# Performance work log

Measured on AMD Instinct MI355X. Metric: run time of the kernel, lower is better.

## Reference

```python
import jax, jax.numpy as jnp
import numpy as np

N = 50000   # nodes
E = 800000  # edges
IND = 128   # in_dim
HID = 128   # num_hidden
NH = 4      # heads
HD = HID // NH
L = 2       # num_layers
SLOPE = 0.2


def setup_inputs() -> dict:
    key = jax.random.key(0)
    ks = jax.random.split(key, 32)
    rn = lambda k, shp, s=1.0: jax.random.normal(k, shp, jnp.float32) * s
    W = 0.08  # weight scale (xavier-ish)
    return {
        "x_t": rn(ks[0], (N, IND)),
        "time_embed": rn(ks[1], (N, HID)),
        "src": jax.random.randint(ks[2], (E,), 0, N),
        "dst": jax.random.randint(ks[3], (E,), 0, N),
        "W_init": rn(ks[4], (IND + HID, HID), W), "b_init": jnp.zeros((HID,), jnp.float32),
        "Wsrc_down": rn(ks[5], (L, HID, HID), W), "bsrc_down": jnp.zeros((L, HID), jnp.float32),
        "Wdst_down": rn(ks[6], (L, HID, HID), W), "bdst_down": jnp.zeros((L, HID), jnp.float32),
        "attn_down": rn(ks[7], (L, NH, HD), W), "bout_down": jnp.zeros((L, HID), jnp.float32),
        "Wsrc_mid": rn(ks[8], (HID, HID), W), "bsrc_mid": jnp.zeros((HID,), jnp.float32),
        "Wdst_mid": rn(ks[9], (HID, HID), W), "bdst_mid": jnp.zeros((HID,), jnp.float32),
        "attn_mid": rn(ks[10], (NH, HD), W), "bout_mid": jnp.zeros((HID,), jnp.float32),
        "Wsrc_up": rn(ks[11], (L, 2 * HID, HID), W), "bsrc_up": jnp.zeros((L, HID), jnp.float32),
        "Wdst_up": rn(ks[12], (L, 2 * HID, HID), W), "bdst_up": jnp.zeros((L, HID), jnp.float32),
        "attn_up": rn(ks[13], (L, NH, HD), W), "bout_up": jnp.zeros((L, HID), jnp.float32),
        "W_fin": rn(ks[14], (HID, HID), W), "b_fin": jnp.zeros((HID,), jnp.float32),
    }


def gatv2_layer(h, Wsrc, bsrc, Wdst, bdst, attn, bout, src, dst):
    # GATv2Conv (DGL semantics, eval mode / no dropout), flatten(1) included.
    fs = (h @ Wsrc + bsrc).reshape(-1, NH, HD)  # [N,H,D]
    fd = (h @ Wdst + bdst).reshape(-1, NH, HD)
    e = jax.nn.leaky_relu(fs[src] + fd[dst], SLOPE)           # [E,H,D]
    logits = jnp.einsum('ehd,hd->eh', e, attn)                # [E,H]
    m = jax.ops.segment_max(logits, dst, num_segments=N)      # [N,H]
    m = jnp.where(jnp.isfinite(m), m, 0.0)                    # zero-in-degree safety
    p = jnp.exp(logits - m[dst])                              # [E,H]
    s = jax.ops.segment_sum(p, dst, num_segments=N)           # [N,H]
    alpha = p / (s[dst] + 1e-9)                               # edge softmax per dst
    out = jax.ops.segment_sum(alpha[:, :, None] * fs[src], dst, num_segments=N)
    out = out.reshape(-1, HID) + bout
    return jax.nn.gelu(out)


def reference(x_t, time_embed, src, dst,
              W_init, b_init,
              Wsrc_down, bsrc_down, Wdst_down, bdst_down, attn_down, bout_down,
              Wsrc_mid, bsrc_mid, Wdst_mid, bdst_mid, attn_mid, bout_mid,
              Wsrc_up, bsrc_up, Wdst_up, bdst_up, attn_up, bout_up,
              W_fin, b_fin):
    h = jnp.concatenate([x_t, time_embed], axis=1)
    h = jax.nn.gelu(h @ W_init + b_init)
    skips = []
    for i in range(L):
        skips.append(h)
        h = gatv2_layer(h, Wsrc_down[i], bsrc_down[i], Wdst_down[i], bdst_down[i],
                        attn_down[i], bout_down[i], src, dst)
    h = gatv2_layer(h, Wsrc_mid, bsrc_mid, Wdst_mid, bdst_mid, attn_mid, bout_mid, src, dst)
    for i in range(L):
        h = jnp.concatenate([h, skips[L - 1 - i]], axis=1)
        h = gatv2_layer(h, Wsrc_up[i], bsrc_up[i], Wdst_up[i], bdst_up[i],
                        attn_up[i], bout_up[i], src, dst)
    out = h @ W_fin + b_fin
    return (out, h)
```

## Files before the change

kernel.cpp:

```cpp
#include <hip/hip_runtime.h>
#include <hip/hip_bf16.h>
#include <math.h>

#define HIDDIM 128

typedef float f32x4 __attribute__((ext_vector_type(4)));
typedef int i32x4 __attribute__((ext_vector_type(4)));
typedef short bf16x8 __attribute__((ext_vector_type(8)));

__device__ inline float gelu_f(float x) {
  float x3 = x * x * x;
  return 0.5f * x * (1.0f + tanhf(0.7978845608028654f * (x + 0.044715f * x3)));
}

__device__ inline void split_bf16(float a, unsigned short& hi, unsigned short& lo) {
  unsigned u = __float_as_uint(a);
  unsigned r = (u + 0x7FFFu + ((u >> 16) & 1u)) & 0xFFFF0000u;
  hi = (unsigned short)(r >> 16);
  float rem = a - __uint_as_float(r);
  unsigned u2 = __float_as_uint(rem);
  lo = (unsigned short)((u2 + 0x7FFFu + ((u2 >> 16) & 1u)) >> 16);
}

__device__ inline void split_pair(float a0, float a1, unsigned& hp, unsigned& lp) {
  unsigned u0 = __float_as_uint(a0), u1 = __float_as_uint(a1);
  unsigned r0 = (u0 + 0x7FFFu + ((u0 >> 16) & 1u)) & 0xFFFF0000u;
  unsigned r1 = (u1 + 0x7FFFu + ((u1 >> 16) & 1u)) & 0xFFFF0000u;
  hp = (r0 >> 16) | r1;
  float m0 = a0 - __uint_as_float(r0);
  float m1 = a1 - __uint_as_float(r1);
  unsigned v0 = __float_as_uint(m0), v1 = __float_as_uint(m1);
  unsigned s0 = v0 + 0x7FFFu + ((v0 >> 16) & 1u);
  unsigned s1 = (v1 + 0x7FFFu + ((v1 >> 16) & 1u)) & 0xFFFF0000u;
  lp = (s0 >> 16) | s1;
}

__global__ void detect_dtype(const unsigned short* __restrict__ raw, int* __restrict__ flag) {
  __shared__ int cnt;
  if (threadIdx.x == 0) cnt = 0;
  __syncthreads();
  int c = 0;
  for (int i = threadIdx.x; i < 8192; i += 256) {
    int ex = (raw[i] >> 7) & 0xFF;
    if (ex >= 0xC0) c++;
  }
  atomicAdd(&cnt, c);
  __syncthreads();
  if (threadIdx.x == 0) flag[0] = (cnt > 64) ? 1 : 0;
}

__global__ void cvt_to_f32_2(const void* __restrict__ in0, const void* __restrict__ in1,
                             float* __restrict__ out0, float* __restrict__ out1,
                             int n, const int* __restrict__ flag) {
  int i = blockIdx.x * 256 + threadIdx.x;
  if (i < n) {
    out0[i] = flag[0] ? ((const float*)in0)[i]
                      : __bfloat162float(((const __hip_bfloat16*)in0)[i]);
  } else if (i < 2 * n) {
    int j = i - n;
    out1[j] = flag[0] ? ((const float*)in1)[j]
                      : __bfloat162float(((const __hip_bfloat16*)in1)[j]);
  }
}

#define NITEMS 14
struct StageArgs {
  const void* src[NITEMS];
  int off[NITEMS];
  int n[NITEMS];
  int blk0[NITEMS];
};
__global__ void stage_params(StageArgs a, float* __restrict__ params,
                             const int* __restrict__ flag) {
  int b = blockIdx.x;
  int it = 0;
  while (it + 1 < NITEMS && a.blk0[it + 1] <= b) ++it;
  int i = (b - a.blk0[it]) * 256 + threadIdx.x;
  if (i < a.n[it]) {
    params[a.off[it] + i] = flag[0]
        ? ((const float*)a.src[it])[i]
        : __bfloat162float(((const __hip_bfloat16*)a.src[it])[i]);
  }
}

#define NSPLIT 12
struct SplitArgs {
  const void* src[NSPLIT];
  int eoff[NSPLIT];
  int soff[NSPLIT];
  int K[NSPLIT];
  int blk0[NSPLIT];
};
__global__ void split_weights(SplitArgs a,
                              unsigned short* __restrict__ whi,
                              unsigned short* __restrict__ wlo,
                              const int* __restrict__ flag) {
  int b = blockIdx.x, it = 0;
  while (it + 1 < NSPLIT && a.blk0[it + 1] <= b) ++it;
  int i = (b - a.blk0[it]) * 256 + threadIdx.x;
  int K = a.K[it];
  if (i < K * 128) {
    float v = flag[0]
        ? ((const float*)a.src[it])[a.eoff[it] + i]
        : __bfloat162float(((const __hip_bfloat16*)a.src[it])[a.eoff[it] + i]);
    int k = i >> 7, col = i & 127;
    unsigned short h, lo;
    split_bf16(v, h, lo);
    int o = a.soff[it] + col * K + k;
    whi[o] = h;
    wlo[o] = lo;
  }
}

template <int FUSED, int FINAL, int ACT, int ACCUM, int KS>
__global__ __launch_bounds__(256, 2) void gemm_ws(
    const float* __restrict__ A,
    const unsigned short* __restrict__ Whi0, const unsigned short* __restrict__ Wlo0,
    const unsigned short* __restrict__ Whi1, const unsigned short* __restrict__ Wlo1,
    const float* __restrict__ b0, const float* __restrict__ b1,
    float* __restrict__ C0, float* __restrict__ C1, int M) {
  constexpr int CT = FUSED ? 4 : 2;
  const int t = threadIdx.x;
  const int w = t >> 6, l = t & 63;
  const int lr = l & 15, lk = l >> 4;
  const unsigned short* whi = Whi0;
  const unsigned short* wlo = Wlo0;
  const float* bw = b0;
  float* Cw = C0;
  int cbase;
  if (FUSED) {
    if (w >> 1) { whi = Whi1; wlo = Wlo1; bw = b1; Cw = C1; }
    cbase = (w & 1) * 64;
  } else {
    cbase = w * 32;
  }

  bf16x8 wh[CT][4], wl[CT][4];
#pragma unroll
  for (int ct = 0; ct < CT; ++ct)
#pragma unroll
    for (int s = 0; s < 4; ++s) {
      size_t off = (size_t)(cbase + ct * 16 + lr) * KS + s * 32 + lk * 8;
      wh[ct][s] = *(const bf16x8*)&whi[off];
      wl[ct][s] = *(const bf16x8*)&wlo[off];
    }

  f32x4 bias[CT];
  if (FINAL) {
#pragma unroll
    for (int ct = 0; ct < CT; ++ct)
      bias[ct] = *(const f32x4*)&bw[cbase + ct * 16 + lk * 4];
  }

  const int ntiles = (M + 31) >> 5;
  for (int tb = blockIdx.x; tb < ntiles; tb += gridDim.x) {
    int row[2];
#pragma unroll
    for (int rt = 0; rt < 2; ++rt) row[rt] = min(tb * 32 + rt * 16 + lr, M - 1);

    float4 raw[2][4][2];
#pragma unroll
    for (int rt = 0; rt < 2; ++rt)
#pragma unroll
      for (int s = 0; s < 4; ++s) {
        const float* ap = &A[(size_t)row[rt] * 128 + s * 32 + lk * 8];
        raw[rt][s][0] = *(const float4*)ap;
        raw[rt][s][1] = *(const float4*)(ap + 4);
      }

    f32x4 acc[2][CT];
#pragma unroll
    for (int rt = 0; rt < 2; ++rt)
#pragma unroll
      for (int ct = 0; ct < CT; ++ct) acc[rt][ct] = (f32x4){0.f, 0.f, 0.f, 0.f};

#pragma unroll
    for (int s = 0; s < 4; ++s) {
      bf16x8 ah[2], al[2];
#pragma unroll
      for (int rt = 0; rt < 2; ++rt) {
        float4 v0 = raw[rt][s][0], v1 = raw[rt][s][1];
        i32x4 hv, lv;
        unsigned hp, lp;
        split_pair(v0.x, v0.y, hp, lp); hv[0] = (int)hp; lv[0] = (int)lp;
        split_pair(v0.z, v0.w, hp, lp); hv[1] = (int)hp; lv[1] = (int)lp;
        split_pair(v1.x, v1.y, hp, lp); hv[2] = (int)hp; lv[2] = (int)lp;
        split_pair(v1.z, v1.w, hp, lp); hv[3] = (int)hp; lv[3] = (int)lp;
        ah[rt] = __builtin_bit_cast(bf16x8, hv);
        al[rt] = __builtin_bit_cast(bf16x8, lv);
      }
#pragma unroll
      for (int rt = 0; rt < 2; ++rt)
#pragma unroll
        for (int ct = 0; ct < CT; ++ct) {
          acc[rt][ct] = __builtin_amdgcn_mfma_f32_16x16x32_bf16(wh[ct][s], ah[rt], acc[rt][ct], 0, 0, 0);
          acc[rt][ct] = __builtin_amdgcn_mfma_f32_16x16x32_bf16(wh[ct][s], al[rt], acc[rt][ct], 0, 0, 0);
          acc[rt][ct] = __builtin_amdgcn_mfma_f32_16x16x32_bf16(wl[ct][s], ah[rt], acc[rt][ct], 0, 0, 0);
        }
    }

#pragma unroll
    for (int rt = 0; rt < 2; ++rt) {
      int r = tb * 32 + rt * 16 + lr;
      if (r < M) {
        float* cp = &Cw[(size_t)r * 128 + cbase + lk * 4];
#pragma unroll
        for (int ct = 0; ct < CT; ++ct) {
          f32x4 v = acc[rt][ct];
          if (ACCUM) v += *(const f32x4*)(cp + ct * 16);
          if (FINAL) v += bias[ct];
          if (ACT) {
            v[0] = gelu_f(v[0]); v[1] = gelu_f(v[1]);
            v[2] = gelu_f(v[2]); v[3] = gelu_f(v[3]);
          }
          *(f32x4*)(cp + ct * 16) = v;
        }
      }
    }
  }
}

__global__ void count_deg(const int* __restrict__ dst, int* __restrict__ deg, int E) {
  int e = blockIdx.x * 256 + threadIdx.x;
  if (e < E) atomicAdd(&deg[dst[e]], 1);
}

__global__ __launch_bounds__(1024) void scan_blocks(
    const int* __restrict__ deg, int* __restrict__ rowptr,
    int* __restrict__ cursor, int* __restrict__ bsum, int N) {
  __shared__ int buf[1024];
  int i = blockIdx.x * 1024 + threadIdx.x;
  int v = (i < N) ? deg[i] : 0;
  buf[threadIdx.x] = v;
  __syncthreads();
  for (int off = 1; off < 1024; off <<= 1) {
    int add = (threadIdx.x >= (unsigned)off) ? buf[threadIdx.x - off] : 0;
    __syncthreads();
    buf[threadIdx.x] += add;
    __syncthreads();
  }
  int excl = buf[threadIdx.x] - v;
  if (i < N) { rowptr[i] = excl; cursor[i] = excl; }
  if (threadIdx.x == 1023) bsum[blockIdx.x] = buf[1023];
}

__global__ __launch_bounds__(1024) void scan_partials(int* __restrict__ bsum, int nb) {
  __shared__ int buf[1024];
  int v = (threadIdx.x < (unsigned)nb) ? bsum[threadIdx.x] : 0;
  buf[threadIdx.x] = v;
  __syncthreads();
  for (int off = 1; off < 1024; off <<= 1) {
    int add = (threadIdx.x >= (unsigned)off) ? buf[threadIdx.x - off] : 0;
    __syncthreads();
    buf[threadIdx.x] += add;
    __syncthreads();
  }
  int excl = buf[threadIdx.x] - v;
  if (threadIdx.x < (unsigned)nb) bsum[threadIdx.x] = excl;
  if (threadIdx.x == 1023) bsum[nb] = buf[1023];
}

__global__ void add_offsets(int* __restrict__ rowptr, int* __restrict__ cursor,
                            const int* __restrict__ bsum, int N, int nb) {
  int i = blockIdx.x * 256 + threadIdx.x;
  if (i < N) {
    int add = bsum[i >> 10];
    rowptr[i] += add;
    cursor[i] += add;
  }
  if (i == 0) rowptr[N] = bsum[nb];
}

__global__ void place_edges(const int* __restrict__ src, const int* __restrict__ dst,
                            int* __restrict__ cursor, int* __restrict__ colsrc, int E) {
  int e = blockIdx.x * 256 + threadIdx.x;
  if (e < E) {
    int pos = atomicAdd(&cursor[dst[e]], 1);
    colsrc[pos] = src[e];
  }
}

__global__ __launch_bounds__(256) void gat_agg(
    const float* __restrict__ fs, const float* __restrict__ fd,
    const int* __restrict__ rowptr, const int* __restrict__ colsrc,
    const float* __restrict__ attn, const float* __restrict__ bout,
    float* __restrict__ hout, int N, int E) {
  int wv = threadIdx.x >> 6, lane = threadIdx.x & 63;
  int n = blockIdx.x * 4 + wv;
  if (n >= N) return;
  int half = lane >> 5;
  int fb = (lane & 31) * 4;
  float4 fdv = *(const float4*)&fd[(size_t)n * HIDDIM + fb];
  float a0 = attn[fb], a1 = attn[fb + 1], a2 = attn[fb + 2], a3 = attn[fb + 3];
  int e0 = rowptr[n], e1 = rowptr[n + 1];
  e0 = max(0, min(e0, E));
  e1 = max(e0, min(e1, E));
  float s = 0.f, ax = 0.f, ay = 0.f, az = 0.f, aw = 0.f;
  for (int c0 = e0; c0 < e1; c0 += 64) {
    int cn = min(64, e1 - c0);
    int myidx = (lane < cn) ? colsrc[c0 + lane] : 0;
    myidx = ((unsigned)myidx < (unsigned)N) ? myidx : 0;
    int iters = (cn + 3) >> 2;
    for (int it = 0; it < iters; ++it) {
      int jA = 4 * it + half;
      int jB = jA + 2;
      int sA = __shfl(myidx, min(jA, cn - 1));
      int sB = __shfl(myidx, min(jB, cn - 1));
      float4 fA = *(const float4*)&fs[(size_t)sA * HIDDIM + fb];
      float4 fB = *(const float4*)&fs[(size_t)sB * HIDDIM + fb];
      float v0, v1, v2, v3, lA, lB;
      v0 = fA.x + fdv.x; v0 = v0 > 0.f ? v0 : 0.2f * v0;
      v1 = fA.y + fdv.y; v1 = v1 > 0.f ? v1 : 0.2f * v1;
      v2 = fA.z + fdv.z; v2 = v2 > 0.f ? v2 : 0.2f * v2;
      v3 = fA.w + fdv.w; v3 = v3 > 0.f ? v3 : 0.2f * v3;
      lA = fmaf(v0, a0, fmaf(v1, a1, fmaf(v2, a2, v3 * a3)));
      v0 = fB.x + fdv.x; v0 = v0 > 0.f ? v0 : 0.2f * v0;
      v1 = fB.y + fdv.y; v1 = v1 > 0.f ? v1 : 0.2f * v1;
      v2 = fB.z + fdv.z; v2 = v2 > 0.f ? v2 : 0.2f * v2;
      v3 = fB.w + fdv.w; v3 = v3 > 0.f ? v3 : 0.2f * v3;
      lB = fmaf(v0, a0, fmaf(v1, a1, fmaf(v2, a2, v3 * a3)));
      lA += __shfl_xor(lA, 1); lA += __shfl_xor(lA, 2); lA += __shfl_xor(lA, 4);
      lB += __shfl_xor(lB, 1); lB += __shfl_xor(lB, 2); lB += __shfl_xor(lB, 4);
      lA = fminf(lA, 60.f);
      lB = fminf(lB, 60.f);
      float pA = (jA < cn) ? __expf(lA) : 0.f;
      float pB = (jB < cn) ? __expf(lB) : 0.f;
      s += pA + pB;
      ax = fmaf(pA, fA.x, fmaf(pB, fB.x, ax));
      ay = fmaf(pA, fA.y, fmaf(pB, fB.y, ay));
      az = fmaf(pA, fA.z, fmaf(pB, fB.z, az));
      aw = fmaf(pA, fA.w, fmaf(pB, fB.w, aw));
    }
  }
  s += __shfl_xor(s, 32);
  ax += __shfl_xor(ax, 32); ay += __shfl_xor(ay, 32);
  az += __shfl_xor(az, 32); aw += __shfl_xor(aw, 32);
  if (half == 0) {
    float inv = 1.f / (s + 1e-9f);
    float o0 = gelu_f(fmaf(ax, inv, bout[fb]));
    float o1 = gelu_f(fmaf(ay, inv, bout[fb + 1]));
    float o2 = gelu_f(fmaf(az, inv, bout[fb + 2]));
    float o3 = gelu_f(fmaf(aw, inv, bout[fb + 3]));
    *(float4*)&hout[(size_t)n * HIDDIM + fb] = make_float4(o0, o1, o2, o3);
  }
}

__global__ void store_out(const float* __restrict__ og, const float* __restrict__ h,
                          void* __restrict__ dout, int n, const int* __restrict__ flag) {
  int i = blockIdx.x * 256 + threadIdx.x;
  if (i >= n) return;
  if (flag[0]) {
    ((float*)dout)[i] = og[i];
    ((float*)dout)[n + i] = h[i];
  } else {
    ((__hip_bfloat16*)dout)[i] = __float2bfloat16(og[i]);
    ((__hip_bfloat16*)dout)[n + i] = __float2bfloat16(h[i]);
  }
}

#define PB_INIT    0
#define PBSRC_DOWN 128
#define PBDST_DOWN 384
#define PATTN_DOWN 640
#define PBOUT_DOWN 896
#define PBSRC_MID  1152
#define PBDST_MID  1280
#define PATTN_MID  1408
#define PBOUT_MID  1536
#define PBSRC_UP   1664
#define PBDST_UP   1920
#define PATTN_UP   2176
#define PBOUT_UP   2432
#define PB_FIN     2688
#define PARAMS_TOTAL 2816

#define SP_W_INIT    0
#define SP_WSRC_D0   32768
#define SP_WSRC_D1   49152
#define SP_WDST_D0   65536
#define SP_WDST_D1   81920
#define SP_WSRC_MID  98304
#define SP_WDST_MID  114688
#define SP_WSRC_U0   131072
#define SP_WSRC_U1   163840
#define SP_WDST_U0   196608
#define SP_WDST_U1   229376
#define SP_W_FIN     262144
#define SPLIT_TOTAL  278528

extern "C" void kernel_launch(void* const* d_in, const int* in_sizes, int n_in,
                              void* d_out, int out_size, void* d_ws, size_t ws_size,
                              hipStream_t stream) {
  const int N = in_sizes[1] / HIDDIM;
  const int E = in_sizes[2];
  const int* src = (const int*)d_in[2];
  const int* dst = (const int*)d_in[3];

  char* p = (char*)d_ws;
  auto carve = [&](size_t bytes) {
    void* r = (void*)p;
    p += (bytes + 255) & ~(size_t)255;
    return r;
  };
  int* flag     = (int*)carve(256);
  float* params = (float*)carve((size_t)PARAMS_TOTAL * 4);
  unsigned short* whi = (unsigned short*)carve((size_t)SPLIT_TOTAL * 2);
  unsigned short* wlo = (unsigned short*)carve((size_t)SPLIT_TOTAL * 2);
  int* deg      = (int*)carve((size_t)N * 4);
  int* rowptr   = (int*)carve((size_t)(N + 1) * 4);
  int* cursor   = (int*)carve((size_t)N * 4);
  int* bsum     = (int*)carve(1032 * 4);
  int* colsrc   = (int*)carve((size_t)E * 4);
  float* hA     = (float*)carve((size_t)N * HIDDIM * 4);
  float* hB     = (float*)carve((size_t)N * HIDDIM * 4);
  float* hC     = (float*)carve((size_t)N * HIDDIM * 4);
  float* fs     = (float*)carve((size_t)N * HIDDIM * 4);
  float* fd     = (float*)carve((size_t)N * HIDDIM * 4);

  detect_dtype<<<1, 256, 0, stream>>>((const unsigned short*)d_in[0], flag);

  static const int idx[NITEMS] = {5, 7, 9, 10, 11, 13, 15, 16, 17, 19, 21, 22, 23, 25};
  static const int off[NITEMS] = {
    PB_INIT, PBSRC_DOWN, PBDST_DOWN, PATTN_DOWN, PBOUT_DOWN,
    PBSRC_MID, PBDST_MID, PATTN_MID, PBOUT_MID,
    PBSRC_UP, PBDST_UP, PATTN_UP, PBOUT_UP, PB_FIN};
  static const int cnt[NITEMS] = {
    128, 256, 256, 256, 256, 128, 128, 128, 128, 256, 256, 256, 256, 128};
  StageArgs sa;
  int nb = 0;
  for (int i = 0; i < NITEMS; ++i) {
    sa.src[i] = d_in[idx[i]];
    sa.off[i] = off[i];
    sa.n[i] = cnt[i];
    sa.blk0[i] = nb;
    nb += (cnt[i] + 255) / 256;
  }
  stage_params<<<nb, 256, 0, stream>>>(sa, params, flag);

  static const int widx[NSPLIT]  = {4, 6, 6, 8, 8, 12, 14, 18, 18, 20, 20, 24};
  static const int weoff[NSPLIT] = {0, 0, 16384, 0, 16384, 0, 0, 0, 32768, 0, 32768, 0};
  static const int wsoff[NSPLIT] = {
    SP_W_INIT, SP_WSRC_D0, SP_WSRC_D1, SP_WDST_D0, SP_WDST_D1,
    SP_WSRC_MID, SP_WDST_MID, SP_WSRC_U0, SP_WSRC_U1, SP_WDST_U0, SP_WDST_U1,
    SP_W_FIN};
  static const int wK[NSPLIT] = {256, 128, 128, 128, 128, 128, 128, 256, 256, 256, 256, 128};
  SplitArgs spa;
  int snb = 0;
  for (int i = 0; i < NSPLIT; ++i) {
    spa.src[i] = d_in[widx[i]];
    spa.eoff[i] = weoff[i];
    spa.soff[i] = wsoff[i];
    spa.K[i] = wK[i];
    spa.blk0[i] = snb;
    snb += (wK[i] * 128 + 255) / 256;
  }
  split_weights<<<snb, 256, 0, stream>>>(spa, whi, wlo, flag);

  float* xc = fs;
  float* tc = fd;
  cvt_to_f32_2<<<(2 * N * HIDDIM + 255) / 256, 256, 0, stream>>>(
      d_in[0], d_in[1], xc, tc, N * HIDDIM, flag);

  hipMemsetAsync(deg, 0, (size_t)N * 4, stream);
  count_deg<<<(E + 255) / 256, 256, 0, stream>>>(dst, deg, E);
  int nsb = (N + 1023) / 1024;
  scan_blocks<<<nsb, 1024, 0, stream>>>(deg, rowptr, cursor, bsum, N);
  scan_partials<<<1, 1024, 0, stream>>>(bsum, nsb);
  add_offsets<<<(N + 255) / 256, 256, 0, stream>>>(rowptr, cursor, bsum, N, nsb);
  place_edges<<<(E + 255) / 256, 256, 0, stream>>>(src, dst, cursor, colsrc, E);

  const int ntiles = (N + 31) >> 5;
  dim3 gw((unsigned)min(512, ntiles));
  dim3 ga((N + 3) / 4);
  const float* P = params;
  const unsigned short* nh = nullptr;

  gemm_ws<0, 0, 0, 0, 256><<<gw, 256, 0, stream>>>(
      xc, whi + SP_W_INIT, wlo + SP_W_INIT, nh, nh,
      nullptr, nullptr, hA, nullptr, N);
  gemm_ws<0, 1, 1, 1, 256><<<gw, 256, 0, stream>>>(
      tc, whi + SP_W_INIT + 128, wlo + SP_W_INIT + 128, nh, nh,
      P + PB_INIT, nullptr, hA, nullptr, N);

  gemm_ws<1, 1, 0, 0, 128><<<gw, 256, 0, stream>>>(
      hA, whi + SP_WSRC_D0, wlo + SP_WSRC_D0, whi + SP_WDST_D0, wlo + SP_WDST_D0,
      P + PBSRC_DOWN, P + PBDST_DOWN, fs, fd, N);
  gat_agg<<<ga, 256, 0, stream>>>(fs, fd, rowptr, colsrc,
                                  P + PATTN_DOWN, P + PBOUT_DOWN, hB, N, E);
  gemm_ws<1, 1, 0, 0, 128><<<gw, 256, 0, stream>>>(
      hB, whi + SP_WSRC_D1, wlo + SP_WSRC_D1, whi + SP_WDST_D1, wlo + SP_WDST_D1,
      P + PBSRC_DOWN + 128, P + PBDST_DOWN + 128, fs, fd, N);
  gat_agg<<<ga, 256, 0, stream>>>(fs, fd, rowptr, colsrc,
                                  P + PATTN_DOWN + 128, P + PBOUT_DOWN + 128, hC, N, E);
  gemm_ws<1, 1, 0, 0, 128><<<gw, 256, 0, stream>>>(
      hC, whi + SP_WSRC_MID, wlo + SP_WSRC_MID, whi + SP_WDST_MID, wlo + SP_WDST_MID,
      P + PBSRC_MID, P + PBDST_MID, fs, fd, N);
  gat_agg<<<ga, 256, 0, stream>>>(fs, fd, rowptr, colsrc,
                                  P + PATTN_MID, P + PBOUT_MID, hC, N, E);
  gemm_ws<1, 0, 0, 0, 256><<<gw, 256, 0, stream>>>(
      hC, whi + SP_WSRC_U0, wlo + SP_WSRC_U0, whi + SP_WDST_U0, wlo + SP_WDST_U0,
      nullptr, nullptr, fs, fd, N);
  gemm_ws<1, 1, 0, 1, 256><<<gw, 256, 0, stream>>>(
      hB, whi + SP_WSRC_U0 + 128, wlo + SP_WSRC_U0 + 128,
      whi + SP_WDST_U0 + 128, wlo + SP_WDST_U0 + 128,
      P + PBSRC_UP, P + PBDST_UP, fs, fd, N);
  gat_agg<<<ga, 256, 0, stream>>>(fs, fd, rowptr, colsrc,
                                  P + PATTN_UP, P + PBOUT_UP, hC, N, E);
  gemm_ws<1, 0, 0, 0, 256><<<gw, 256, 0, stream>>>(
      hC, whi + SP_WSRC_U1, wlo + SP_WSRC_U1, whi + SP_WDST_U1, wlo + SP_WDST_U1,
      nullptr, nullptr, fs, fd, N);
  gemm_ws<1, 1, 0, 1, 256><<<gw, 256, 0, stream>>>(
      hA, whi + SP_WSRC_U1 + 128, wlo + SP_WSRC_U1 + 128,
      whi + SP_WDST_U1 + 128, wlo + SP_WDST_U1 + 128,
      P + PBSRC_UP + 128, P + PBDST_UP + 128, fs, fd, N);
  gat_agg<<<ga, 256, 0, stream>>>(fs, fd, rowptr, colsrc,
                                  P + PATTN_UP + 128, P + PBOUT_UP + 128, hC, N, E);

  float* outg = hB;
  gemm_ws<0, 1, 0, 0, 128><<<gw, 256, 0, stream>>>(
      hC, whi + SP_W_FIN, wlo + SP_W_FIN, nh, nh,
      P + PB_FIN, nullptr, outg, nullptr, N);
  store_out<<<(N * HIDDIM + 255) / 256, 256, 0, stream>>>(outg, hC, d_out, N * HIDDIM, flag);
}
```

Baseline: 921.4 us.

## Split GEMM over a 2D grid, prefetch A in halves, simplify GATv2 leaky-relu

The GEMM kernel no longer runs a persistent grid-stride loop in which one block fuses the src and dst matrices. It launches one block per 32-row tile, with blockIdx.y selecting the src or dst weight matrix. Each wave now holds only 2 column tiles of weights, so register pressure drops and the launch bound rises to 3 blocks per SM. A is loaded two k-slices at a time, with the next slices prefetched while the current ones are converted. In gat_agg, leaky-relu plus the attention dot becomes 0.6*a*x + 0.4*a*|x|, and the shuffle index clamp is dropped. The trade-off is that each weight fragment is reloaded per tile, and A is read twice across the two matrix blocks.

```diff
diff --git a/kernel.cpp b/kernel.cpp
--- a/kernel.cpp
+++ b/kernel.cpp
@@ -112,32 +112,41 @@
   }
 }
 
-template <int FUSED, int FINAL, int ACT, int ACCUM, int KS>
-__global__ __launch_bounds__(256, 2) void gemm_ws(
+template <int FINAL, int ACT, int ACCUM, int KS>
+__global__ __launch_bounds__(256, 3) void gemm_ws(
     const float* __restrict__ A,
     const unsigned short* __restrict__ Whi0, const unsigned short* __restrict__ Wlo0,
     const unsigned short* __restrict__ Whi1, const unsigned short* __restrict__ Wlo1,
     const float* __restrict__ b0, const float* __restrict__ b1,
     float* __restrict__ C0, float* __restrict__ C1, int M) {
-  constexpr int CT = FUSED ? 4 : 2;
   const int t = threadIdx.x;
   const int w = t >> 6, l = t & 63;
   const int lr = l & 15, lk = l >> 4;
-  const unsigned short* whi = Whi0;
-  const unsigned short* wlo = Wlo0;
-  const float* bw = b0;
-  float* Cw = C0;
-  int cbase;
-  if (FUSED) {
-    if (w >> 1) { whi = Whi1; wlo = Wlo1; bw = b1; Cw = C1; }
-    cbase = (w & 1) * 64;
-  } else {
-    cbase = w * 32;
-  }
-
-  bf16x8 wh[CT][4], wl[CT][4];
-#pragma unroll
-  for (int ct = 0; ct < CT; ++ct)
+  const int mat = blockIdx.y;
+  const unsigned short* whi = mat ? Whi1 : Whi0;
+  const unsigned short* wlo = mat ? Wlo1 : Wlo0;
+  const float* bw = mat ? b1 : b0;
+  float* Cw = mat ? C1 : C0;
+  const int cbase = w * 32;
+  const int tb = blockIdx.x;
+
+  int row[2];
+#pragma unroll
+  for (int rt = 0; rt < 2; ++rt) row[rt] = min(tb * 32 + rt * 16 + lr, M - 1);
+
+  float4 rA[2][2][2];
+#pragma unroll
+  for (int s = 0; s < 2; ++s)
+#pragma unroll
+    for (int rt = 0; rt < 2; ++rt) {
+      const float* ap = &A[(size_t)row[rt] * 128 + s * 32 + lk * 8];
+      rA[s][rt][0] = *(const float4*)ap;
+      rA[s][rt][1] = *(const float4*)(ap + 4);
+    }
+
+  bf16x8 wh[2][4], wl[2][4];
+#pragma unroll
+  for (int ct = 0; ct < 2; ++ct)
 #pragma unroll
     for (int s = 0; s < 4; ++s) {
       size_t off = (size_t)(cbase + ct * 16 + lr) * KS + s * 32 + lk * 8;
@@ -145,76 +154,68 @@
       wl[ct][s] = *(const bf16x8*)&wlo[off];
     }
 
-  f32x4 bias[CT];
+  f32x4 bias[2];
   if (FINAL) {
 #pragma unroll
-    for (int ct = 0; ct < CT; ++ct)
+    for (int ct = 0; ct < 2; ++ct)
       bias[ct] = *(const f32x4*)&bw[cbase + ct * 16 + lk * 4];
   }
 
-  const int ntiles = (M + 31) >> 5;
-  for (int tb = blockIdx.x; tb < ntiles; tb += gridDim.x) {
-    int row[2];
-#pragma unroll
-    for (int rt = 0; rt < 2; ++rt) row[rt] = min(tb * 32 + rt * 16 + lr, M - 1);
-
-    float4 raw[2][4][2];
+  f32x4 acc[2][2];
+#pragma unroll
+  for (int rt = 0; rt < 2; ++rt)
+#pragma unroll
+    for (int ct = 0; ct < 2; ++ct) acc[rt][ct] = (f32x4){0.f, 0.f, 0.f, 0.f};
+
+#pragma unroll
+  for (int s = 0; s < 4; ++s) {
+    const int cur = s & 1;
+    bf16x8 ah[2], al[2];
+#pragma unroll
+    for (int rt = 0; rt < 2; ++rt) {
+      float4 v0 = rA[cur][rt][0], v1 = rA[cur][rt][1];
+      i32x4 hv, lv;
+      unsigned hp, lp;
+      split_pair(v0.x, v0.y, hp, lp); hv[0] = (int)hp; lv[0] = (int)lp;
+      split_pair(v0.z, v0.w, hp, lp); hv[1] = (int)hp; lv[1] = (int)lp;
+      split_pair(v1.x, v1.y, hp, lp); hv[2] = (int)hp; lv[2] = (int)lp;
+      split_pair(v1.z, v1.w, hp, lp); hv[3] = (int)hp; lv[3] = (int)lp;
+      ah[rt] = __builtin_bit_cast(bf16x8, hv);
+      al[rt] = __builtin_bit_cast(bf16x8, lv);
+    }
+    if (s + 2 < 4) {
+#pragma unroll
+      for (int rt = 0; rt < 2; ++rt) {
+        const float* ap = &A[(size_t)row[rt] * 128 + (s + 2) * 32 + lk * 8];
+        rA[cur][rt][0] = *(const float4*)ap;
+        rA[cur][rt][1] = *(const float4*)(ap + 4);
+      }
+    }
 #pragma unroll
     for (int rt = 0; rt < 2; ++rt)
 #pragma unroll
-      for (int s = 0; s < 4; ++s) {
-        const float* ap = &A[(size_t)row[rt] * 128 + s * 32 + lk * 8];
-        raw[rt][s][0] = *(const float4*)ap;
-        raw[rt][s][1] = *(const float4*)(ap + 4);
+      for (int ct = 0; ct < 2; ++ct) {
+        acc[rt][ct] = __builtin_amdgcn_mfma_f32_16x16x32_bf16(wh[ct][s], ah[rt], acc[rt][ct], 0, 0, 0);
+        acc[rt][ct] = __builtin_amdgcn_mfma_f32_16x16x32_bf16(wh[ct][s], al[rt], acc[rt][ct], 0, 0, 0);
+        acc[rt][ct] = __builtin_amdgcn_mfma_f32_16x16x32_bf16(wl[ct][s], ah[rt], acc[rt][ct], 0, 0, 0);
       }
-
-    f32x4 acc[2][CT];
-#pragma unroll
-    for (int rt = 0; rt < 2; ++rt)
-#pragma unroll
-      for (int ct = 0; ct < CT; ++ct) acc[rt][ct] = (f32x4){0.f, 0.f, 0.f, 0.f};
-
-#pragma unroll
-    for (int s = 0; s < 4; ++s) {
-      bf16x8 ah[2], al[2];
-#pragma unroll
-      for (int rt = 0; rt < 2; ++rt) {
-        float4 v0 = raw[rt][s][0], v1 = raw[rt][s][1];
-        i32x4 hv, lv;
-        unsigned hp, lp;
-        split_pair(v0.x, v0.y, hp, lp); hv[0] = (int)hp; lv[0] = (int)lp;
-        split_pair(v0.z, v0.w, hp, lp); hv[1] = (int)hp; lv[1] = (int)lp;
-        split_pair(v1.x, v1.y, hp, lp); hv[2] = (int)hp; lv[2] = (int)lp;
-        split_pair(v1.z, v1.w, hp, lp); hv[3] = (int)hp; lv[3] = (int)lp;
-        ah[rt] = __builtin_bit_cast(bf16x8, hv);
-        al[rt] = __builtin_bit_cast(bf16x8, lv);
-      }
-#pragma unroll
-      for (int rt = 0; rt < 2; ++rt)
-#pragma unroll
-        for (int ct = 0; ct < CT; ++ct) {
-          acc[rt][ct] = __builtin_amdgcn_mfma_f32_16x16x32_bf16(wh[ct][s], ah[rt], acc[rt][ct], 0, 0, 0);
-          acc[rt][ct] = __builtin_amdgcn_mfma_f32_16x16x32_bf16(wh[ct][s], al[rt], acc[rt][ct], 0, 0, 0);
-          acc[rt][ct] = __builtin_amdgcn_mfma_f32_16x16x32_bf16(wl[ct][s], ah[rt], acc[rt][ct], 0, 0, 0);
+  }
+
+#pragma unroll
+  for (int rt = 0; rt < 2; ++rt) {
+    int r = tb * 32 + rt * 16 + lr;
+    if (r < M) {
+      float* cp = &Cw[(size_t)r * 128 + cbase + lk * 4];
+#pragma unroll
+      for (int ct = 0; ct < 2; ++ct) {
+        f32x4 v = acc[rt][ct];
+        if (ACCUM) v += *(const f32x4*)(cp + ct * 16);
+        if (FINAL) v += bias[ct];
+        if (ACT) {
+          v[0] = gelu_f(v[0]); v[1] = gelu_f(v[1]);
+          v[2] = gelu_f(v[2]); v[3] = gelu_f(v[3]);
         }
-    }
-
-#pragma unroll
-    for (int rt = 0; rt < 2; ++rt) {
-      int r = tb * 32 + rt * 16 + lr;
-      if (r < M) {
-        float* cp = &Cw[(size_t)r * 128 + cbase + lk * 4];
-#pragma unroll
-        for (int ct = 0; ct < CT; ++ct) {
-          f32x4 v = acc[rt][ct];
-          if (ACCUM) v += *(const f32x4*)(cp + ct * 16);
-          if (FINAL) v += bias[ct];
-          if (ACT) {
-            v[0] = gelu_f(v[0]); v[1] = gelu_f(v[1]);
-            v[2] = gelu_f(v[2]); v[3] = gelu_f(v[3]);
-          }
-          *(f32x4*)(cp + ct * 16) = v;
-        }
+        *(f32x4*)(cp + ct * 16) = v;
       }
     }
   }
@@ -291,7 +292,9 @@
   int half = lane >> 5;
   int fb = (lane & 31) * 4;
   float4 fdv = *(const float4*)&fd[(size_t)n * HIDDIM + fb];
-  float a0 = attn[fb], a1 = attn[fb + 1], a2 = attn[fb + 2], a3 = attn[fb + 3];
+  float b0_ = attn[fb], b1_ = attn[fb + 1], b2_ = attn[fb + 2], b3_ = attn[fb + 3];
+  float a60 = 0.6f * b0_, a61 = 0.6f * b1_, a62 = 0.6f * b2_, a63 = 0.6f * b3_;
+  float a40 = 0.4f * b0_, a41 = 0.4f * b1_, a42 = 0.4f * b2_, a43 = 0.4f * b3_;
   int e0 = rowptr[n], e1 = rowptr[n + 1];
   e0 = max(0, min(e0, E));
   e1 = max(e0, min(e1, E));
@@ -304,21 +307,21 @@
     for (int it = 0; it < iters; ++it) {
       int jA = 4 * it + half;
       int jB = jA + 2;
-      int sA = __shfl(myidx, min(jA, cn - 1));
-      int sB = __shfl(myidx, min(jB, cn - 1));
+      int sA = __shfl(myidx, jA);
+      int sB = __shfl(myidx, jB);
       float4 fA = *(const float4*)&fs[(size_t)sA * HIDDIM + fb];
       float4 fB = *(const float4*)&fs[(size_t)sB * HIDDIM + fb];
-      float v0, v1, v2, v3, lA, lB;
-      v0 = fA.x + fdv.x; v0 = v0 > 0.f ? v0 : 0.2f * v0;
-      v1 = fA.y + fdv.y; v1 = v1 > 0.f ? v1 : 0.2f * v1;
-      v2 = fA.z + fdv.z; v2 = v2 > 0.f ? v2 : 0.2f * v2;
-      v3 = fA.w + fdv.w; v3 = v3 > 0.f ? v3 : 0.2f * v3;
-      lA = fmaf(v0, a0, fmaf(v1, a1, fmaf(v2, a2, v3 * a3)));
-      v0 = fB.x + fdv.x; v0 = v0 > 0.f ? v0 : 0.2f * v0;
-      v1 = fB.y + fdv.y; v1 = v1 > 0.f ? v1 : 0.2f * v1;
-      v2 = fB.z + fdv.z; v2 = v2 > 0.f ? v2 : 0.2f * v2;
-      v3 = fB.w + fdv.w; v3 = v3 > 0.f ? v3 : 0.2f * v3;
-      lB = fmaf(v0, a0, fmaf(v1, a1, fmaf(v2, a2, v3 * a3)));
+      float x0, x1, x2, x3, lA, lB;
+      x0 = fA.x + fdv.x; x1 = fA.y + fdv.y; x2 = fA.z + fdv.z; x3 = fA.w + fdv.w;
+      lA = fmaf(a60, x0, a40 * fabsf(x0));
+      lA = fmaf(a61, x1, fmaf(a41, fabsf(x1), lA));
+      lA = fmaf(a62, x2, fmaf(a42, fabsf(x2), lA));
+      lA = fmaf(a63, x3, fmaf(a43, fabsf(x3), lA));
+      x0 = fB.x + fdv.x; x1 = fB.y + fdv.y; x2 = fB.z + fdv.z; x3 = fB.w + fdv.w;
+      lB = fmaf(a60, x0, a40 * fabsf(x0));
+      lB = fmaf(a61, x1, fmaf(a41, fabsf(x1), lB));
+      lB = fmaf(a62, x2, fmaf(a42, fabsf(x2), lB));
+      lB = fmaf(a63, x3, fmaf(a43, fabsf(x3), lB));
       lA += __shfl_xor(lA, 1); lA += __shfl_xor(lA, 2); lA += __shfl_xor(lA, 4);
       lB += __shfl_xor(lB, 1); lB += __shfl_xor(lB, 2); lB += __shfl_xor(lB, 4);
       lA = fminf(lA, 60.f);
@@ -469,47 +472,47 @@
   add_offsets<<<(N + 255) / 256, 256, 0, stream>>>(rowptr, cursor, bsum, N, nsb);
   place_edges<<<(E + 255) / 256, 256, 0, stream>>>(src, dst, cursor, colsrc, E);
 
-  const int ntiles = (N + 31) >> 5;
-  dim3 gw((unsigned)min(512, ntiles));
+  const int nt32 = (N + 31) >> 5;
+  dim3 g1(nt32, 1), g2(nt32, 2);
   dim3 ga((N + 3) / 4);
   const float* P = params;
   const unsigned short* nh = nullptr;
 
-  gemm_ws<0, 0, 0, 0, 256><<<gw, 256, 0, stream>>>(
+  gemm_ws<0, 0, 0, 256><<<g1, 256, 0, stream>>>(
       xc, whi + SP_W_INIT, wlo + SP_W_INIT, nh, nh,
       nullptr, nullptr, hA, nullptr, N);
-  gemm_ws<0, 1, 1, 1, 256><<<gw, 256, 0, stream>>>(
+  gemm_ws<1, 1, 1, 256><<<g1, 256, 0, stream>>>(
       tc, whi + SP_W_INIT + 128, wlo + SP_W_INIT + 128, nh, nh,
       P + PB_INIT, nullptr, hA, nullptr, N);
 
-  gemm_ws<1, 1, 0, 0, 128><<<gw, 256, 0, stream>>>(
+  gemm_ws<1, 0, 0, 128><<<g2, 256, 0, stream>>>(
       hA, whi + SP_WSRC_D0, wlo + SP_WSRC_D0, whi + SP_WDST_D0, wlo + SP_WDST_D0,
       P + PBSRC_DOWN, P + PBDST_DOWN, fs, fd, N);
   gat_agg<<<ga, 256, 0, stream>>>(fs, fd, rowptr, colsrc,
                                   P + PATTN_DOWN, P + PBOUT_DOWN, hB, N, E);
-  gemm_ws<1, 1, 0, 0, 128><<<gw, 256, 0, stream>>>(
+  gemm_ws<1, 0, 0, 128><<<g2, 256, 0, stream>>>(
       hB, whi + SP_WSRC_D1, wlo + SP_WSRC_D1, whi + SP_WDST_D1, wlo + SP_WDST_D1,
       P + PBSRC_DOWN + 128, P + PBDST_DOWN + 128, fs, fd, N);
   gat_agg<<<ga, 256, 0, stream>>>(fs, fd, rowptr, colsrc,
                                   P + PATTN_DOWN + 128, P + PBOUT_DOWN + 128, hC, N, E);
-  gemm_ws<1, 1, 0, 0, 128><<<gw, 256, 0, stream>>>(
+  gemm_ws<1, 0, 0, 128><<<g2, 256, 0, stream>>>(
       hC, whi + SP_WSRC_MID, wlo + SP_WSRC_MID, whi + SP_WDST_MID, wlo + SP_WDST_MID,
       P + PBSRC_MID, P + PBDST_MID, fs, fd, N);
   gat_agg<<<ga, 256, 0, stream>>>(fs, fd, rowptr, colsrc,
                                   P + PATTN_MID, P + PBOUT_MID, hC, N, E);
-  gemm_ws<1, 0, 0, 0, 256><<<gw, 256, 0, stream>>>(
+  gemm_ws<0, 0, 0, 256><<<g2, 256, 0, stream>>>(
       hC, whi + SP_WSRC_U0, wlo + SP_WSRC_U0, whi + SP_WDST_U0, wlo + SP_WDST_U0,
       nullptr, nullptr, fs, fd, N);
-  gemm_ws<1, 1, 0, 1, 256><<<gw, 256, 0, stream>>>(
+  gemm_ws<1, 0, 1, 256><<<g2, 256, 0, stream>>>(
       hB, whi + SP_WSRC_U0 + 128, wlo + SP_WSRC_U0 + 128,
       whi + SP_WDST_U0 + 128, wlo + SP_WDST_U0 + 128,
       P + PBSRC_UP, P + PBDST_UP, fs, fd, N);
   gat_agg<<<ga, 256, 0, stream>>>(fs, fd, rowptr, colsrc,
                                   P + PATTN_UP, P + PBOUT_UP, hC, N, E);
-  gemm_ws<1, 0, 0, 0, 256><<<gw, 256, 0, stream>>>(
+  gemm_ws<0, 0, 0, 256><<<g2, 256, 0, stream>>>(
       hC, whi + SP_WSRC_U1, wlo + SP_WSRC_U1, whi + SP_WDST_U1, wlo + SP_WDST_U1,
       nullptr, nullptr, fs, fd, N);
-  gemm_ws<1, 1, 0, 1, 256><<<gw, 256, 0, stream>>>(
+  gemm_ws<1, 0, 1, 256><<<g2, 256, 0, stream>>>(
       hA, whi + SP_WSRC_U1 + 128, wlo + SP_WSRC_U1 + 128,
       whi + SP_WDST_U1 + 128, wlo + SP_WDST_U1 + 128,
       P + PBSRC_UP + 128, P + PBDST_UP + 128, fs, fd, N);
@@ -517,7 +520,7 @@
                                   P + PATTN_UP + 128, P + PBOUT_UP + 128, hC, N, E);
 
   float* outg = hB;
-  gemm_ws<0, 1, 0, 0, 128><<<gw, 256, 0, stream>>>(
+  gemm_ws<1, 0, 0, 128><<<g1, 256, 0, stream>>>(
       hC, whi + SP_W_FIN, wlo + SP_W_FIN, nh, nh,
       P + PB_FIN, nullptr, outg, nullptr, N);
   store_out<<<(N * HIDDIM + 255) / 256, 256, 0, stream>>>(outg, hC, d_out, N * HIDDIM, flag);
```

Result: slower. 1.058 ms (+14.9%).
